# Kernel optimization log

Measured on AMD Instinct MI355X. Metric: run time of the kernel, lower is better.

The kernel has to match this reference:

```python
import jax, jax.numpy as jnp
from jax import lax
import numpy as np

MAX_ITERS = 20  # module hardcodes self.max_iters = 20


def setup_inputs() -> dict:
    key = jax.random.key(0)
    k1, k2 = jax.random.split(key)
    B, H, W, C, K = 16, 96, 96, 256, 21
    x = jax.random.normal(k1, (B, H, W, C), dtype=jnp.float32)
    N = H * W
    init_idx = jax.random.randint(k2, (B, K), 0, N, dtype=jnp.int64)
    return {"x": x, "init_idx": init_idx}


def _kmeans(x_flat, init_idx):
    # x_flat: [B, N, C]; init_idx: [B, K]
    B, N, C = x_flat.shape
    K = init_idx.shape[1]
    # initial centroids: gather K points per batch
    cent0 = jnp.take_along_axis(x_flat, init_idx[..., None], axis=1)  # [B, K, C]
    x_sq = jnp.sum(x_flat * x_flat, axis=-1, keepdims=True)  # [B, N, 1] (constant term)

    def step(cent, _):
        d = x_sq - 2.0 * jnp.einsum('bnc,bkc->bnk', x_flat, cent) \
            + jnp.sum(cent * cent, axis=-1)[:, None, :]  # [B, N, K]
        assign = jnp.argmin(d, axis=-1)  # [B, N]
        onehot = jax.nn.one_hot(assign, K, dtype=x_flat.dtype)  # [B, N, K]
        sums = jnp.einsum('bnk,bnc->bkc', onehot, x_flat)  # scatter-add
        counts = jnp.sum(onehot, axis=1)  # [B, K]
        # scatter-mean; keep previous centroid for empty clusters
        new_cent = jnp.where(counts[..., None] > 0,
                             sums / jnp.maximum(counts, 1.0)[..., None],
                             cent)
        return new_cent, None

    cent, _ = lax.scan(step, cent0, None, length=MAX_ITERS)
    return cent  # [B, K, C]


def reference(x, init_idx):
    B, H, W, C = x.shape
    x_flat = x.reshape(B, H * W, C)
    return _kmeans(x_flat, init_idx)
```

## Files before the change

### kernel.cpp

```cpp
#include <hip/hip_runtime.h>


#define BB 16
#define NN 9216
#define CC 256
#define KK 21
#define ITERS 20
#define QTR 2304

__device__ __forceinline__ float mul_sep(float a, float b) {
  float t = a * b;
  asm("" : "+v"(t));
  return t;
}

__device__ float np_half_sq(const float* v) {
  float r[8];
  #pragma unroll
  for (int j = 0; j < 8; ++j) r[j] = mul_sep(v[j], v[j]);
  for (int i = 8; i < 128; i += 8) {
    #pragma unroll
    for (int j = 0; j < 8; ++j) r[j] = __fadd_rn(r[j], mul_sep(v[i + j], v[i + j]));
  }
  return __fadd_rn(__fadd_rn(__fadd_rn(r[0], r[1]), __fadd_rn(r[2], r[3])),
                   __fadd_rn(__fadd_rn(r[4], r[5]), __fadd_rn(r[6], r[7])));
}

__global__ __launch_bounds__(512) void decode_idx(
    const void* __restrict__ raw, int* __restrict__ out) {
  __shared__ int all_ok;
  if (threadIdx.x == 0) all_ok = 1;
  __syncthreads();
  const long long* p64 = (const long long*)raw;
  const int* p32 = (const int*)raw;
  int t = threadIdx.x;
  long long v64 = 0;
  if (t < BB * KK) {
    v64 = p64[t];
    if (v64 < 0 || v64 >= NN) atomicAnd(&all_ok, 0);
  }
  __syncthreads();
  if (t < BB * KK) out[t] = all_ok ? (int)v64 : p32[t];
}

__global__ __launch_bounds__(256) void gather_init(
    const float* __restrict__ x, const int* __restrict__ idx_dec,
    float* __restrict__ cent, float* __restrict__ csq) {
  __shared__ float row[CC];
  int bk = blockIdx.x;
  int b = bk / KK;
  int c = threadIdx.x;
  int idx = idx_dec[bk];
  float v = x[((size_t)b * NN + idx) * CC + c];
  cent[(size_t)bk * CC + c] = v;
  row[c] = v;
  __syncthreads();
  if (threadIdx.x == 0)
    csq[bk] = __fadd_rn(np_half_sq(row), np_half_sq(row + 128));
}

__global__ __launch_bounds__(256) void assign_np(
    const float* __restrict__ x, const float* __restrict__ cent,
    const float* __restrict__ csq, int* __restrict__ assign) {
  const int nb = NN / 256;
  int b = blockIdx.x / nb;
  int n = (blockIdx.x % nb) * 256 + threadIdx.x;
  const float* xp = x + ((size_t)b * NN + n) * CC;
  const float* cp = cent + (size_t)b * KK * CC;
  const float* cq = csq + b * KK;

  float q[KK][4];
  #pragma unroll
  for (int k = 0; k < KK; ++k)
    #pragma unroll
    for (int j = 0; j < 4; ++j) q[k][j] = 0.f;
  float rA[8], rB[8];
  #pragma unroll
  for (int j = 0; j < 8; ++j) { rA[j] = 0.f; rB[j] = 0.f; }

#define CHUNK16(C0, R)                                                        \
  do {                                                                        \
    float xv[16];                                                             \
    {                                                                         \
      float4 t0 = *(const float4*)(xp + (C0));                                \
      float4 t1 = *(const float4*)(xp + (C0) + 4);                            \
      float4 t2 = *(const float4*)(xp + (C0) + 8);                            \
      float4 t3 = *(const float4*)(xp + (C0) + 12);                           \
      xv[0] = t0.x; xv[1] = t0.y; xv[2] = t0.z; xv[3] = t0.w;                 \
      xv[4] = t1.x; xv[5] = t1.y; xv[6] = t1.z; xv[7] = t1.w;                 \
      xv[8] = t2.x; xv[9] = t2.y; xv[10] = t2.z; xv[11] = t2.w;               \
      xv[12] = t3.x; xv[13] = t3.y; xv[14] = t3.z; xv[15] = t3.w;             \
    }                                                                         \
    _Pragma("unroll")                                                         \
    for (int g = 0; g < 16; g += 8) {                                         \
      _Pragma("unroll")                                                       \
      for (int j = 0; j < 8; ++j)                                             \
        R[j] = __fadd_rn(R[j], mul_sep(xv[g + j], xv[g + j]));                \
    }                                                                         \
    _Pragma("unroll")                                                         \
    for (int k = 0; k < KK; ++k) {                                            \
      const float* cpk = cp + k * CC + (C0);        \
      _Pragma("unroll")                                                       \
      for (int g2 = 0; g2 < 16; g2 += 4) {                                    \
        _Pragma("unroll")                                                     \
        for (int j = 0; j < 4; ++j)                                           \
          q[k][j] = __fadd_rn(q[k][j], mul_sep(xv[g2 + j], cpk[g2 + j]));     \
      }                                                                       \
    }                                                                         \
  } while (0)

  for (int c0 = 0; c0 < 128; c0 += 16) CHUNK16(c0, rA);
  for (int c0 = 128; c0 < 256; c0 += 16) CHUNK16(c0, rB);
#undef CHUNK16

  float hA = __fadd_rn(__fadd_rn(__fadd_rn(rA[0], rA[1]), __fadd_rn(rA[2], rA[3])),
                       __fadd_rn(__fadd_rn(rA[4], rA[5]), __fadd_rn(rA[6], rA[7])));
  float hB = __fadd_rn(__fadd_rn(__fadd_rn(rB[0], rB[1]), __fadd_rn(rB[2], rB[3])),
                       __fadd_rn(__fadd_rn(rB[4], rB[5]), __fadd_rn(rB[6], rB[7])));
  float xsq = __fadd_rn(hA, hB);

  float best = INFINITY;
  int bestk = 0;
  #pragma unroll
  for (int k = 0; k < KK; ++k) {
    float dk = __fadd_rn(__fadd_rn(q[k][0], q[k][2]), __fadd_rn(q[k][1], q[k][3]));
    float d = __fadd_rn(__fsub_rn(xsq, __fmul_rn(2.0f, dk)), cq[k]);
    if (d < best) { best = d; bestk = k; }
  }
  assign[(size_t)b * NN + n] = bestk;
}

__global__ __launch_bounds__(256) void compact_np(
    const int* __restrict__ assign, int* __restrict__ lists,
    int* __restrict__ counts) {
  __shared__ int idx_lds[4][QTR];
  __shared__ int wcnt[4];
  int bk = blockIdx.x;
  int b = bk / KK, k = bk % KK;
  int lane = threadIdx.x & 63, w = threadIdx.x >> 6;

  const int* ap = assign + (size_t)b * NN + w * QTR;
  int cnt = 0;
  for (int i = 0; i < QTR; i += 64) {
    int a = ap[i + lane];
    unsigned long long m = __ballot(a == k);
    if (a == k) {
      int pos = cnt + (int)__popcll(m & ((1ull << lane) - 1ull));
      idx_lds[w][pos] = w * QTR + i + lane;
    }
    cnt += (int)__popcll(m);
  }
  if (lane == 0) wcnt[w] = cnt;
  __syncthreads();

  int base = 0;
  #pragma unroll
  for (int ww = 0; ww < 4; ++ww) if (ww < w) base += wcnt[ww];
  int* gl = lists + (size_t)bk * NN;
  for (int i = lane; i < cnt; i += 64) gl[base + i] = idx_lds[w][i];
  if (threadIdx.x == 0)
    counts[bk] = wcnt[0] + wcnt[1] + wcnt[2] + wcnt[3];
}

__global__ __launch_bounds__(64) void update_gather(
    const float* __restrict__ x, const int* __restrict__ lists,
    const int* __restrict__ counts, float* __restrict__ cent) {
  int blk = blockIdx.x;
  int bk = blk >> 2, g = blk & 3;
  int b = bk / KK;
  int c = g * 64 + threadIdx.x;
  int total = counts[bk];
  const int* lst = lists + (size_t)bk * NN;
  const float* xb = x + (size_t)b * NN * CC + c;

  float s = 0.f;
  if (total > 0) {
    int i = 0;
    for (; i + 16 <= total; i += 16) {
      int nn[16];
      float v[16];
      #pragma unroll
      for (int j = 0; j < 16; ++j) nn[j] = lst[i + j];
      #pragma unroll
      for (int j = 0; j < 16; ++j) v[j] = xb[(size_t)nn[j] * CC];
      #pragma unroll
      for (int j = 0; j < 16; ++j) s = __fadd_rn(s, v[j]);
    }
    if (i < total) {
      int rem = total - i;
      int nn[16];
      float v[16];
      #pragma unroll
      for (int j = 0; j < 16; ++j) nn[j] = lst[(j < rem) ? (i + j) : i];
      #pragma unroll
      for (int j = 0; j < 16; ++j) v[j] = xb[(size_t)nn[j] * CC];
      #pragma unroll
      for (int j = 0; j < 16; ++j)
        if (j < rem) s = __fadd_rn(s, v[j]);
    }
  }

  float old = cent[(size_t)bk * CC + c];
  float dv = s / fmaxf((float)total, 1.0f);
  float nc = (total > 0) ? dv : old;
  cent[(size_t)bk * CC + c] = nc;
}

__global__ __launch_bounds__(256) void csq_np(
    const float* __restrict__ cent, float* __restrict__ csq) {
  __shared__ float row[CC];
  int bk = blockIdx.x;
  row[threadIdx.x] = cent[(size_t)bk * CC + threadIdx.x];
  __syncthreads();
  if (threadIdx.x == 0)
    csq[bk] = __fadd_rn(np_half_sq(row), np_half_sq(row + 128));
}

extern "C" void kernel_launch(void* const* d_in, const int* in_sizes, int n_in,
                              void* d_out, int out_size, void* d_ws, size_t ws_size,
                              hipStream_t stream) {
  const float* x = (const float*)d_in[0];
  float* cent = (float*)d_out;

  char* ws = (char*)d_ws;
  int* lists = (int*)ws;
  int* assign = lists + (size_t)BB * KK * NN;
  int* counts = assign + (size_t)BB * NN;
  float* csq = (float*)(counts + BB * KK);
  int* idx_dec = (int*)(csq + BB * KK);

  decode_idx<<<1, 512, 0, stream>>>(d_in[1], idx_dec);
  gather_init<<<BB * KK, 256, 0, stream>>>(x, idx_dec, cent, csq);
  for (int it = 0; it < ITERS; ++it) {
    assign_np<<<BB * (NN / 256), 256, 0, stream>>>(x, cent, csq, assign);
    compact_np<<<BB * KK, 256, 0, stream>>>(assign, lists, counts);
    update_gather<<<BB * KK * 4, 64, 0, stream>>>(x, lists, counts, cent);
    csq_np<<<BB * KK, 256, 0, stream>>>(cent, csq);
  }
}
```

Before: 3.839 ms.

## Stage cluster index list in LDS and double-buffer 64-wide gathers in update

```diff
diff --git a/kernel.cpp b/kernel.cpp
--- a/kernel.cpp
+++ b/kernel.cpp
@@ -165,6 +165,7 @@
 __global__ __launch_bounds__(64) void update_gather(
     const float* __restrict__ x, const int* __restrict__ lists,
     const int* __restrict__ counts, float* __restrict__ cent) {
+  __shared__ int lst_lds[NN];
   int blk = blockIdx.x;
   int bk = blk >> 2, g = blk & 3;
   int b = bk / KK;
@@ -173,31 +174,47 @@
   const int* lst = lists + (size_t)bk * NN;
   const float* xb = x + (size_t)b * NN * CC + c;
 
+  for (int i = threadIdx.x; i < total; i += 64) lst_lds[i] = lst[i];
+  __syncthreads();
+
   float s = 0.f;
-  if (total > 0) {
-    int i = 0;
-    for (; i + 16 <= total; i += 16) {
-      int nn[16];
-      float v[16];
+  int nfull = total >> 6;
+  int rem = total & 63;
+
+  float va[64], vb[64];
+  if (nfull > 0) {
+    #pragma unroll
+    for (int j = 0; j < 64; ++j) va[j] = xb[(size_t)lst_lds[j] * CC];
+  }
+  int t = 0;
+  while (t + 2 <= nfull) {
+    #pragma unroll
+    for (int j = 0; j < 64; ++j) vb[j] = xb[(size_t)lst_lds[(t + 1) * 64 + j] * CC];
+    #pragma unroll
+    for (int j = 0; j < 64; ++j) s = __fadd_rn(s, va[j]);
+    if (t + 2 < nfull) {
       #pragma unroll
-      for (int j = 0; j < 16; ++j) nn[j] = lst[i + j];
-      #pragma unroll
-      for (int j = 0; j < 16; ++j) v[j] = xb[(size_t)nn[j] * CC];
-      #pragma unroll
-      for (int j = 0; j < 16; ++j) s = __fadd_rn(s, v[j]);
+      for (int j = 0; j < 64; ++j) va[j] = xb[(size_t)lst_lds[(t + 2) * 64 + j] * CC];
     }
-    if (i < total) {
-      int rem = total - i;
-      int nn[16];
-      float v[16];
-      #pragma unroll
-      for (int j = 0; j < 16; ++j) nn[j] = lst[(j < rem) ? (i + j) : i];
-      #pragma unroll
-      for (int j = 0; j < 16; ++j) v[j] = xb[(size_t)nn[j] * CC];
-      #pragma unroll
-      for (int j = 0; j < 16; ++j)
-        if (j < rem) s = __fadd_rn(s, v[j]);
+    #pragma unroll
+    for (int j = 0; j < 64; ++j) s = __fadd_rn(s, vb[j]);
+    t += 2;
+  }
+  if (t < nfull) {
+    #pragma unroll
+    for (int j = 0; j < 64; ++j) s = __fadd_rn(s, va[j]);
+  }
+  if (rem > 0) {
+    int base = nfull << 6;
+    int dummy = lst_lds[base];
+    #pragma unroll
+    for (int j = 0; j < 64; ++j) {
+      int idx = (j < rem) ? lst_lds[base + j] : dummy;
+      vb[j] = xb[(size_t)idx * CC];
     }
+    #pragma unroll
+    for (int j = 0; j < 64; ++j)
+      if (j < rem) s = __fadd_rn(s, vb[j]);
   }
 
   float old = cent[(size_t)bk * CC + c];
```

After: 3.513 ms. -8.5%, faster.
